# Performance work log

Measured on AMD Instinct MI355X. Metric: run time of the kernel, lower is better.

## Reference

```python
import jax, jax.numpy as jnp
import numpy as np
import math

D_MODEL = 1024
NUM_HEADS = 16
D_HEAD = D_MODEL // NUM_HEADS
BATCH = 2
SEQ = 2048
ROPE_BASE = 10000.0


def get_rotary_embedding(seq_len, d_head):
    # standard RoPE tables: cos/sin of shape [seq_len, d_head]
    inv_freq = 1.0 / (ROPE_BASE ** (jnp.arange(0, d_head, 2, dtype=jnp.float32) / d_head))
    t = jnp.arange(seq_len, dtype=jnp.float32)
    freqs = jnp.outer(t, inv_freq)                      # [S, d_head/2]
    emb = jnp.concatenate([freqs, freqs], axis=-1)      # [S, d_head]
    return jnp.cos(emb), jnp.sin(emb)


def rotate_half(x):
    x1, x2 = jnp.split(x, 2, axis=-1)
    return jnp.concatenate([-x2, x1], axis=-1)


def apply_rotary_pos_emb(x, cos, sin):
    # x: [B, H, S, Dh]; cos/sin: [S, Dh] broadcast over B, H
    return x * cos[None, None, :, :] + rotate_half(x) * sin[None, None, :, :]


def setup_inputs() -> dict:
    key = jax.random.key(0)
    ks = jax.random.split(key, 9)
    s = 1.0 / math.sqrt(D_MODEL)
    inp = {
        "x":  jax.random.normal(ks[0], (BATCH, SEQ, D_MODEL), dtype=jnp.float32),
        "Wq": jax.random.uniform(ks[1], (D_MODEL, D_MODEL), jnp.float32, -s, s),
        "bq": jnp.zeros((D_MODEL,), jnp.float32),
        "Wk": jax.random.uniform(ks[2], (D_MODEL, D_MODEL), jnp.float32, -s, s),
        "bk": jnp.zeros((D_MODEL,), jnp.float32),
        "Wv": jax.random.uniform(ks[3], (D_MODEL, D_MODEL), jnp.float32, -s, s),
        "bv": jnp.zeros((D_MODEL,), jnp.float32),
        "Wo": jax.random.uniform(ks[4], (D_MODEL, D_MODEL), jnp.float32, -s, s),
        "bo": jnp.zeros((D_MODEL,), jnp.float32),
    }
    return inp


def reference(x, Wq, bq, Wk, bk, Wv, bv, Wo, bo) -> jnp.ndarray:
    B, S, _ = x.shape
    H, Dh = NUM_HEADS, D_HEAD

    def proj(W, b):
        y = jnp.einsum('bsd,ed->bse', x, W) + b          # nn.Linear: x @ W^T + b
        return y.reshape(B, S, H, Dh).transpose(0, 2, 1, 3)  # [B,H,S,Dh]

    Q = proj(Wq, bq)
    K = proj(Wk, bk)
    V = proj(Wv, bv)

    cos, sin = get_rotary_embedding(S, Dh)
    Q = apply_rotary_pos_emb(Q, cos, sin)
    K = apply_rotary_pos_emb(K, cos, sin)

    scores = jnp.einsum('bhqd,bhkd->bhqk', Q, K) / math.sqrt(Dh)  # [B,H,S,S]
    causal = jnp.tril(jnp.ones((S, S), dtype=bool))
    scores = jnp.where(causal[None, None, :, :], scores, -jnp.inf)
    attn = jax.nn.softmax(scores, axis=-1)
    # dropout is identity in eval / p=0
    context = jnp.einsum('bhqk,bhkd->bhqd', attn, V)               # [B,H,S,Dh]
    context = context.transpose(0, 2, 1, 3).reshape(B, S, H * Dh)
    return jnp.einsum('bsd,ed->bse', context, Wo) + bo
```

## Files before the change

kernel.cpp:

```cpp
#include <hip/hip_runtime.h>
#include <hip/hip_bf16.h>
#include <math.h>

typedef __attribute__((ext_vector_type(8))) short short8;
typedef __attribute__((ext_vector_type(8))) __bf16 bf16x8;
typedef __attribute__((ext_vector_type(4))) float f32x4;
typedef __attribute__((ext_vector_type(16))) float f32x16;

#define D_MODEL 1024
#define NUM_HEADS 16
#define D_HEAD 64
#define BATCH 2
#define SEQ 2048
#define BH (BATCH * NUM_HEADS)
#define MTOT (BATCH * SEQ)

__device__ inline f32x4 mfma16(short8 a, short8 b, f32x4 c) {
  return __builtin_amdgcn_mfma_f32_16x16x32_bf16(
      __builtin_bit_cast(bf16x8, a), __builtin_bit_cast(bf16x8, b), c, 0, 0, 0);
}

__device__ inline f32x16 mfma32(short8 a, short8 b, f32x16 c) {
  return __builtin_amdgcn_mfma_f32_32x32x16_bf16(
      __builtin_bit_cast(bf16x8, a), __builtin_bit_cast(bf16x8, b), c, 0, 0, 0);
}

__device__ inline unsigned short f2b(float f) {
  __hip_bfloat16 h = __float2bfloat16(f);
  return __builtin_bit_cast(unsigned short, h);
}

__device__ inline unsigned cvt_pk_bf16(float lo, float hi) {
  unsigned r;
  asm("v_cvt_pk_bf16_f32 %0, %1, %2" : "=v"(r) : "v"(lo), "v"(hi));
  return r;
}

__device__ inline float exp2_hw(float x) {
  float r;
  asm("v_exp_f32 %0, %1" : "=v"(r) : "v"(x));
  return r;
}

__device__ inline void permlane32_swap(unsigned& a, unsigned& b) {
  asm("v_permlane32_swap_b32 %0, %1" : "+v"(a), "+v"(b));
}

__device__ __forceinline__ void wait_barrier_vm0() {
  asm volatile("s_waitcnt vmcnt(0)\n\ts_barrier" ::: "memory");
}

#define GLOAD_LDS16(gaddr, laddr)                                              \
  __builtin_amdgcn_global_load_lds(                                            \
      (const __attribute__((address_space(1))) void*)(gaddr),                  \
      (__attribute__((address_space(3))) void*)(laddr), 16, 0, 0)

__global__ void cvt_f32_bf16(const float* __restrict__ in,
                             unsigned short* __restrict__ out, int n) {
  int i = (blockIdx.x * 256 + threadIdx.x) * 4;
  if (i >= n) return;
  float4 v = *(const float4*)(in + i);
  ushort4 o;
  o.x = f2b(v.x); o.y = f2b(v.y); o.z = f2b(v.z); o.w = f2b(v.w);
  *(ushort4*)(out + i) = o;
}

__global__ void cvt4_f32_bf16(const float* __restrict__ w0, const float* __restrict__ w1,
                              const float* __restrict__ w2, const float* __restrict__ w3,
                              unsigned short* __restrict__ o0, unsigned short* __restrict__ o1,
                              unsigned short* __restrict__ o2, unsigned short* __restrict__ o3,
                              int n) {
  const float* in; unsigned short* out;
  switch (blockIdx.y) {
    case 0: in = w0; out = o0; break;
    case 1: in = w1; out = o1; break;
    case 2: in = w2; out = o2; break;
    default: in = w3; out = o3; break;
  }
  int i = (blockIdx.x * 256 + threadIdx.x) * 4;
  if (i >= n) return;
  float4 v = *(const float4*)(in + i);
  ushort4 o;
  o.x = f2b(v.x); o.y = f2b(v.y); o.z = f2b(v.z); o.w = f2b(v.w);
  *(ushort4*)(out + i) = o;
}

__global__ void trig_kernel(float2* __restrict__ tct) {
  int idx = blockIdx.x * 256 + threadIdx.x;
  int i = idx & 31;
  int s = idx >> 5;
  float inv = powf(10000.0f, -(float)i / 32.0f);
  float t = (float)s * inv;
  tct[idx] = make_float2(cosf(t), sinf(t));
}

#define STAGE64(t, bufi)                                                        \
  do {                                                                          \
    const int _k0 = (t) * 64;                                                   \
    const int _gc = ((lane & 7) ^ (lane >> 3)) * 8;                             \
    const int _lc = (lane & 7) * 8;                                             \
    for (int j = 0; j < 4; j++) {                                               \
      const int _r = w * 32 + j * 8 + (lane >> 3);                              \
      GLOAD_LDS16(&A[(size_t)(bm + _r) * D_MODEL + _k0 + _gc], &As[bufi][_r][_lc]); \
      GLOAD_LDS16(&Bp[(size_t)(bn + _r) * D_MODEL + _k0 + _gc], &Bs[bufi][_r][_lc]); \
    }                                                                           \
  } while (0)

#define KLOOP64()                                                               \
  do {                                                                          \
    const int NT = D_MODEL / 64;                                                \
    STAGE64(0, 0);                                                              \
    for (int t = 0; t < NT; ++t) {                                              \
      const int cur = t & 1;                                                    \
      wait_barrier_vm0();                                                       \
      if (t + 1 < NT) STAGE64(t + 1, cur ^ 1);                                  \
      for (int kk = 0; kk < 2; kk++) {                                          \
        short8 af[4], bf4[4];                                                   \
        for (int mi = 0; mi < 4; mi++)                                          \
          af[mi] = *(const short8*)&As[cur][wr + mi * 16 + fr]                  \
                                         [(kk * 32 + fk) ^ ((fr & 7) << 3)];    \
        for (int ni = 0; ni < 4; ni++)                                          \
          bf4[ni] = *(const short8*)&Bs[cur][wc + ni * 16 + fr]                 \
                                          [(kk * 32 + fk) ^ ((fr & 7) << 3)];   \
        __builtin_amdgcn_s_setprio(1);                                          \
        for (int mi = 0; mi < 4; mi++)                                          \
          for (int ni = 0; ni < 4; ni++)                                        \
            acc[mi][ni] = mfma16(af[mi], bf4[ni], acc[mi][ni]);                 \
        __builtin_amdgcn_s_setprio(0);                                          \
      }                                                                         \
    }                                                                           \
  } while (0)

__global__ __launch_bounds__(256) void gemm_qkv(
    const unsigned short* __restrict__ A,
    const unsigned short* __restrict__ Bp,
    const float* __restrict__ bq, const float* __restrict__ bk,
    const float* __restrict__ bv,
    const float2* __restrict__ tct,
    unsigned short* __restrict__ Qb, unsigned short* __restrict__ Kb,
    unsigned short* __restrict__ Vt) {
  __shared__ unsigned short As[2][128][64];
  __shared__ unsigned short Bs[2][128][64];
  const int bm = blockIdx.y * 128;
  const int bn = blockIdx.x * 128;
  const int tid = threadIdx.x;
  const int lane = tid & 63;
  const int w = tid >> 6;
  const int wr = (w >> 1) * 64, wc = (w & 1) * 64;
  const int fr = lane & 15;
  const int g = lane >> 4;
  const int fk = g * 8;

  f32x4 acc[4][4] = {};
  KLOOP64();

  const int type = bn >> 10;
  const int cloc = (bn & 1023) + wc;
  if (type <= 1) {
    const float* bias = (type == 0) ? bq : bk;
    unsigned short* outp = (type == 0) ? Qb : Kb;
    const float SC = (type == 0) ? 0.125f * 1.44269504f : 1.0f;
    const int h = cloc >> 6;
    for (int mi = 0; mi < 4; mi++)
      for (int r = 0; r < 4; r++) {
        int row = bm + wr + mi * 16 + g * 4 + r;
        int b = row >> 11, s = row & (SEQ - 1);
        size_t base = (((size_t)(b * NUM_HEADS + h)) * SEQ + s) * 64;
        for (int ni = 0; ni < 2; ni++) {
          int i = ni * 16 + fr;
          float x0 = acc[mi][ni][r] + bias[cloc + i];
          float x1 = acc[mi][ni + 2][r] + bias[cloc + i + 32];
          float2 cs = tct[s * 32 + i];
          outp[base + i]      = f2b((x0 * cs.x - x1 * cs.y) * SC);
          outp[base + i + 32] = f2b((x1 * cs.x + x0 * cs.y) * SC);
        }
      }
  } else {
    for (int mi = 0; mi < 4; mi++) {
      int row0 = bm + wr + mi * 16 + g * 4;
      int b = row0 >> 11, s0 = row0 & (SEQ - 1);
      for (int ni = 0; ni < 4; ni++) {
        int col = cloc + ni * 16 + fr;
        int h = col >> 6, dh = col & 63;
        float bvv = bv[col];
        uint2 pk = make_uint2(
            cvt_pk_bf16(acc[mi][ni][0] + bvv, acc[mi][ni][1] + bvv),
            cvt_pk_bf16(acc[mi][ni][2] + bvv, acc[mi][ni][3] + bvv));
        *(uint2*)&Vt[(((size_t)(b * NUM_HEADS + h)) * 64 + dh) * SEQ + s0] = pk;
      }
    }
  }
}

__global__ __launch_bounds__(256) void gemm_out(
    const unsigned short* __restrict__ A,
    const unsigned short* __restrict__ Bp,
    const float* __restrict__ bias,
    float* __restrict__ outf) {
  __shared__ unsigned short As[2][128][64];
  __shared__ unsigned short Bs[2][128][64];
  const int bm = blockIdx.y * 128;
  const int bn = blockIdx.x * 128;
  const int tid = threadIdx.x;
  const int lane = tid & 63;
  const int w = tid >> 6;
  const int wr = (w >> 1) * 64, wc = (w & 1) * 64;
  const int fr = lane & 15;
  const int g = lane >> 4;
  const int fk = g * 8;

  f32x4 acc[4][4] = {};
  KLOOP64();

  for (int mi = 0; mi < 4; mi++)
    for (int ni = 0; ni < 4; ni++)
      for (int r = 0; r < 4; r++) {
        int row = bm + wr + mi * 16 + g * 4 + r;
        int col = bn + wc + ni * 16 + fr;
        outf[(size_t)row * D_MODEL + col] = acc[mi][ni][r] + bias[col];
      }
}

__global__ __launch_bounds__(256) void flash_attn(
    const unsigned short* __restrict__ Q,
    const unsigned short* __restrict__ Km,
    const unsigned short* __restrict__ Vt,
    unsigned short* __restrict__ ctx) {
  __shared__ unsigned short Ks[2][64 * 64];
  __shared__ unsigned short Vs[2][64 * 64];
  const int bh = blockIdx.x;
  const int by = blockIdx.y;
  const int qt = (by < 8) ? (15 - by) : (by - 8);
  const int tid = threadIdx.x;
  const int lane = tid & 63;
  const int w = tid >> 6;
  const int q31 = lane & 31;
  const int hi = lane >> 5;

  const unsigned short* Qp = Q + (size_t)bh * SEQ * 64;
  const unsigned short* Kp = Km + (size_t)bh * SEQ * 64;
  const unsigned short* Vp = Vt + (size_t)bh * 64 * SEQ;
  const int b = bh >> 4, h = bh & 15;

  const int qbase = qt * 128;
  const int qrow0 = qbase + w * 32;
  const int wmax = qrow0 + 31;
  const int q = qrow0 + q31;

  short8 qf[4];
  for (int s = 0; s < 4; s++)
    qf[s] = *(const short8*)&Qp[(size_t)q * 64 + s * 16 + hi * 8];

  const int srow = tid >> 2;
  const int ss0 = (tid & 3) * 2, ss1 = ss0 + 1;
  const int lw0 = srow * 64 + ((ss0 ^ (srow & 7)) * 8);
  const int lw1 = srow * 64 + ((ss1 ^ (srow & 7)) * 8);

  short8 krA = *(const short8*)&Kp[(size_t)srow * 64 + ss0 * 8];
  short8 krB = *(const short8*)&Kp[(size_t)srow * 64 + ss1 * 8];
  short8 vrA = *(const short8*)&Vp[(size_t)srow * SEQ + ss0 * 8];
  short8 vrB = *(const short8*)&Vp[(size_t)srow * SEQ + ss1 * 8];

  f32x16 oacc0 = {}, oacc1 = {};
  float lq = 0.f;
  const int NSTEPS = 2 * qt + 2;

  for (int step = 0; step < NSTEPS; ++step) {
    const int kbase = step * 64;
    const int cur = step & 1;
    *(short8*)&Ks[cur][lw0] = krA;
    *(short8*)&Ks[cur][lw1] = krB;
    *(short8*)&Vs[cur][lw0] = vrA;
    *(short8*)&Vs[cur][lw1] = vrB;
    __syncthreads();
    if (step + 1 < NSTEPS) {
      const int nk = kbase + 64;
      krA = *(const short8*)&Kp[(size_t)(nk + srow) * 64 + ss0 * 8];
      krB = *(const short8*)&Kp[(size_t)(nk + srow) * 64 + ss1 * 8];
      vrA = *(const short8*)&Vp[(size_t)srow * SEQ + nk + ss0 * 8];
      vrB = *(const short8*)&Vp[(size_t)srow * SEQ + nk + ss1 * 8];
    }

    if (kbase <= wmax) {
      for (int kt = 0; kt < 2; kt++) {
        const int ktb = kbase + kt * 32;
        if (ktb <= wmax) {
          f32x16 sacc = {};
          const int krow = kt * 32 + q31;
          const int kro = krow * 64;
          const int ksw = krow & 7;
          for (int s = 0; s < 4; s++) {
            short8 kf = *(const short8*)&Ks[cur][kro + (((s * 2 + hi) ^ ksw) * 8)];
            sacc = mfma32(kf, qf[s], sacc);
          }
          const bool maskT = (ktb + 31 > qrow0);
          float p[16];
          float rs = 0.f;
#pragma unroll
          for (int reg = 0; reg < 16; reg++) {
            float sv = sacc[reg];
            if (maskT) {
              int key = ktb + (reg & 3) + 8 * (reg >> 2) + 4 * hi;
              sv = (key <= q) ? sv : -INFINITY;
            }
            p[reg] = exp2_hw(sv);
            rs += p[reg];
          }
          lq += rs;
          short8 paf[2];
#pragma unroll
          for (int sl = 0; sl < 2; sl++) {
            const int o = sl * 8;
            unsigned a0 = cvt_pk_bf16(p[o + 0], p[o + 1]);
            unsigned b0 = cvt_pk_bf16(p[o + 4], p[o + 5]);
            permlane32_swap(a0, b0);
            unsigned a1 = cvt_pk_bf16(p[o + 2], p[o + 3]);
            unsigned b1 = cvt_pk_bf16(p[o + 6], p[o + 7]);
            permlane32_swap(a1, b1);
            uint4 u = make_uint4(a0, a1, b0, b1);
            paf[sl] = __builtin_bit_cast(short8, u);
          }
#pragma unroll
          for (int dt = 0; dt < 2; dt++) {
            const int vrow = dt * 32 + q31;
            const int vro = vrow * 64;
            const int vsw = vrow & 7;
#pragma unroll
            for (int sl = 0; sl < 2; sl++) {
              short8 vf = *(const short8*)&Vs[cur][vro + (((kt * 4 + sl * 2 + hi) ^ vsw) * 8)];
              if (dt == 0) oacc0 = mfma32(paf[sl], vf, oacc0);
              else         oacc1 = mfma32(paf[sl], vf, oacc1);
            }
          }
        }
      }
    }
  }

  lq += __shfl_xor(lq, 32);
#pragma unroll
  for (int reg = 0; reg < 16; reg++) {
    const int crow = (reg & 3) + 8 * (reg >> 2) + 4 * hi;
    const float linv = 1.f / __shfl(lq, crow);
    const int row = qrow0 + crow;
    size_t base = ((size_t)b * SEQ + row) * D_MODEL + h * 64 + q31;
    ctx[base]      = f2b(oacc0[reg] * linv);
    ctx[base + 32] = f2b(oacc1[reg] * linv);
  }
}

extern "C" void kernel_launch(void* const* d_in, const int* in_sizes, int n_in,
                              void* d_out, int out_size, void* d_ws, size_t ws_size,
                              hipStream_t stream) {
  const float* x  = (const float*)d_in[0];
  const float* Wq = (const float*)d_in[1];
  const float* bq = (const float*)d_in[2];
  const float* Wk = (const float*)d_in[3];
  const float* bk = (const float*)d_in[4];
  const float* Wv = (const float*)d_in[5];
  const float* bv = (const float*)d_in[6];
  const float* Wo = (const float*)d_in[7];
  const float* bo = (const float*)d_in[8];
  float* out = (float*)d_out;

  char* ws = (char*)d_ws;
  size_t off = 0;
  auto alloc = [&](size_t bytes) {
    char* p = ws + off;
    off += (bytes + 255) & ~(size_t)255;
    return p;
  };
  unsigned short* xb   = (unsigned short*)alloc((size_t)MTOT * D_MODEL * 2);
  unsigned short* wqkv = (unsigned short*)alloc((size_t)3 * D_MODEL * D_MODEL * 2);
  unsigned short* wob  = (unsigned short*)alloc((size_t)D_MODEL * D_MODEL * 2);
  unsigned short* Qb   = (unsigned short*)alloc((size_t)BH * SEQ * 64 * 2);
  unsigned short* Kb   = (unsigned short*)alloc((size_t)BH * SEQ * 64 * 2);
  unsigned short* Vt   = (unsigned short*)alloc((size_t)BH * 64 * SEQ * 2);
  unsigned short* ctxb = (unsigned short*)alloc((size_t)MTOT * D_MODEL * 2);
  float2* tct = (float2*)alloc((size_t)SEQ * 32 * 8);

  int nx = MTOT * D_MODEL;
  int nw = D_MODEL * D_MODEL;
  cvt_f32_bf16<<<nx / 1024, 256, 0, stream>>>(x, xb, nx);
  cvt4_f32_bf16<<<dim3(nw / 1024, 4), 256, 0, stream>>>(
      Wq, Wk, Wv, Wo, wqkv, wqkv + nw, wqkv + 2 * (size_t)nw, wob, nw);
  trig_kernel<<<SEQ * 32 / 256, 256, 0, stream>>>(tct);

  gemm_qkv<<<dim3(3 * D_MODEL / 128, MTOT / 128), 256, 0, stream>>>(
      xb, wqkv, bq, bk, bv, tct, Qb, Kb, Vt);

  flash_attn<<<dim3(BH, 16), 256, 0, stream>>>(Qb, Kb, Vt, ctxb);

  gemm_out<<<dim3(D_MODEL / 128, MTOT / 128), 256, 0, stream>>>(ctxb, wob, bo, out);
}
```

Before: 121.2 us.

## Pair causal query tiles in one 512-thread block to share K/V staging

```diff
diff --git a/kernel.cpp b/kernel.cpp
--- a/kernel.cpp
+++ b/kernel.cpp
@@ -221,7 +221,7 @@
       }
 }
 
-__global__ __launch_bounds__(256) void flash_attn(
+__global__ __launch_bounds__(512) void flash_attn(
     const unsigned short* __restrict__ Q,
     const unsigned short* __restrict__ Km,
     const unsigned short* __restrict__ Vt,
@@ -230,10 +230,11 @@
   __shared__ unsigned short Vs[2][64 * 64];
   const int bh = blockIdx.x;
   const int by = blockIdx.y;
-  const int qt = (by < 8) ? (15 - by) : (by - 8);
   const int tid = threadIdx.x;
   const int lane = tid & 63;
   const int w = tid >> 6;
+  const int gi = w >> 2;
+  const int wl = w & 3;
   const int q31 = lane & 31;
   const int hi = lane >> 5;
 
@@ -242,8 +243,9 @@
   const unsigned short* Vp = Vt + (size_t)bh * 64 * SEQ;
   const int b = bh >> 4, h = bh & 15;
 
+  const int qt = gi ? by : (15 - by);
   const int qbase = qt * 128;
-  const int qrow0 = qbase + w * 32;
+  const int qrow0 = qbase + wl * 32;
   const int wmax = qrow0 + 31;
   const int q = qrow0 + q31;
 
@@ -251,34 +253,27 @@
   for (int s = 0; s < 4; s++)
     qf[s] = *(const short8*)&Qp[(size_t)q * 64 + s * 16 + hi * 8];
 
-  const int srow = tid >> 2;
-  const int ss0 = (tid & 3) * 2, ss1 = ss0 + 1;
-  const int lw0 = srow * 64 + ((ss0 ^ (srow & 7)) * 8);
-  const int lw1 = srow * 64 + ((ss1 ^ (srow & 7)) * 8);
-
-  short8 krA = *(const short8*)&Kp[(size_t)srow * 64 + ss0 * 8];
-  short8 krB = *(const short8*)&Kp[(size_t)srow * 64 + ss1 * 8];
-  short8 vrA = *(const short8*)&Vp[(size_t)srow * SEQ + ss0 * 8];
-  short8 vrB = *(const short8*)&Vp[(size_t)srow * SEQ + ss1 * 8];
+  const int srow = tid >> 3;
+  const int ss = tid & 7;
+  const int lw = srow * 64 + ((ss ^ (srow & 7)) * 8);
+
+  short8 kr = *(const short8*)&Kp[(size_t)srow * 64 + ss * 8];
+  short8 vr = *(const short8*)&Vp[(size_t)srow * SEQ + ss * 8];
 
   f32x16 oacc0 = {}, oacc1 = {};
   float lq = 0.f;
-  const int NSTEPS = 2 * qt + 2;
+  const int NSTEPS = 2 * (15 - by) + 2;
 
   for (int step = 0; step < NSTEPS; ++step) {
     const int kbase = step * 64;
     const int cur = step & 1;
-    *(short8*)&Ks[cur][lw0] = krA;
-    *(short8*)&Ks[cur][lw1] = krB;
-    *(short8*)&Vs[cur][lw0] = vrA;
-    *(short8*)&Vs[cur][lw1] = vrB;
+    *(short8*)&Ks[cur][lw] = kr;
+    *(short8*)&Vs[cur][lw] = vr;
     __syncthreads();
     if (step + 1 < NSTEPS) {
       const int nk = kbase + 64;
-      krA = *(const short8*)&Kp[(size_t)(nk + srow) * 64 + ss0 * 8];
-      krB = *(const short8*)&Kp[(size_t)(nk + srow) * 64 + ss1 * 8];
-      vrA = *(const short8*)&Vp[(size_t)srow * SEQ + nk + ss0 * 8];
-      vrB = *(const short8*)&Vp[(size_t)srow * SEQ + nk + ss1 * 8];
+      kr = *(const short8*)&Kp[(size_t)(nk + srow) * 64 + ss * 8];
+      vr = *(const short8*)&Vp[(size_t)srow * SEQ + nk + ss * 8];
     }
 
     if (kbase <= wmax) {
@@ -389,7 +384,7 @@
   gemm_qkv<<<dim3(3 * D_MODEL / 128, MTOT / 128), 256, 0, stream>>>(
       xb, wqkv, bq, bk, bv, tct, Qb, Kb, Vt);
 
-  flash_attn<<<dim3(BH, 16), 256, 0, stream>>>(Qb, Kb, Vt, ctxb);
+  flash_attn<<<dim3(BH, 8), 512, 0, stream>>>(Qb, Kb, Vt, ctxb);
 
   gemm_out<<<dim3(D_MODEL / 128, MTOT / 128), 256, 0, stream>>>(ctxb, wob, bo, out);
 }
```

New measurement: 118.4 us. 1.02x faster.
